# Optimization experiments

Hardware: AMD Instinct MI355X
Metric: run time of the kernel (lower is better)

The kernel has to match this reference:

```python
import jax, jax.numpy as jnp
import numpy as np

GROUPS = 3
EPS = 1e-5

def _conv(x, w, groups, pad):
    # x: NCHW, w: OIHW (grouped). pad: 'VALID' for 1x1, ((1,1),(1,1)) for 3x3 same.
    return jax.lax.conv_general_dilated(
        x, w, window_strides=(1, 1), padding=pad,
        feature_group_count=groups,
        dimension_numbers=('NCHW', 'OIHW', 'NCHW'))

def _bn(x, g, b, m, v):
    # folded inference batchnorm: y = x*scale + (beta - mean*scale)
    s = g / jnp.sqrt(v + EPS)
    return x * s[None, :, None, None] + (b - m * s)[None, :, None, None]

def _shuffle(x, groups):
    B, C, H, W = x.shape
    return x.reshape(B, groups, C // groups, H, W).transpose(0, 2, 1, 3, 4).reshape(B, C, H, W)

def setup_inputs() -> dict:
    key = jax.random.key(0)
    ks = jax.random.split(key, 16)
    B, Cin, Cout, H, W = 64, 480, 480, 28, 28
    mid = Cout // 4  # 120
    d = {}
    d['x'] = jax.random.normal(ks[0], (B, Cin, H, W), jnp.float32)
    d['w1'] = jax.random.normal(ks[1], (mid, Cin // GROUPS, 1, 1), jnp.float32) * 0.05
    d['g1'] = jax.random.uniform(ks[2], (mid,), jnp.float32)
    d['b1'] = jax.random.normal(ks[3], (mid,), jnp.float32)
    d['m1'] = jax.random.normal(ks[4], (mid,), jnp.float32)
    d['v1'] = jax.random.uniform(ks[5], (mid,), jnp.float32)
    d['w2'] = jax.random.normal(ks[6], (mid, 1, 3, 3), jnp.float32) * 0.05
    d['g2'] = jax.random.uniform(ks[7], (mid,), jnp.float32)
    d['b2'] = jax.random.normal(ks[8], (mid,), jnp.float32)
    d['m2'] = jax.random.normal(ks[9], (mid,), jnp.float32)
    d['v2'] = jax.random.uniform(ks[10], (mid,), jnp.float32)
    d['w3'] = jax.random.normal(ks[11], (Cout, mid // GROUPS, 1, 1), jnp.float32) * 0.05
    d['g3'] = jax.random.uniform(ks[12], (Cout,), jnp.float32)
    d['b3'] = jax.random.normal(ks[13], (Cout,), jnp.float32)
    d['m3'] = jax.random.normal(ks[14], (Cout,), jnp.float32)
    d['v3'] = jax.random.uniform(ks[15], (Cout,), jnp.float32)
    return d

def reference(x, w1, g1, b1, m1, v1, w2, g2, b2, m2, v2, w3, g3, b3, m3, v3):
    mid = w2.shape[0]
    shortcut = x  # in_channels == out_channels -> identity shortcut
    out = jax.nn.relu(_bn(_conv(x, w1, GROUPS, 'VALID'), g1, b1, m1, v1))
    out = _bn(_conv(out, w2, mid, ((1, 1), (1, 1))), g2, b2, m2, v2)  # depthwise 3x3
    out = _shuffle(out, GROUPS)
    out = jax.nn.relu(_bn(_conv(out, w3, GROUPS, 'VALID'), g3, b3, m3, v3))
    return out + shortcut
```

## Files before the change

kernel.cpp:

```cpp
#include <hip/hip_runtime.h>


namespace {
constexpr int CIN = 480;
constexpr int MID = 120;
constexpr int HWP = 784;
constexpr float EPSV = 1e-5f;

constexpr size_t TMP1_N = (size_t)64 * MID * HWP;
constexpr int WA1_N = 3 * 3 * 5 * 64 * 8;
constexpr int WA3_N = 3 * 10 * 2 * 64 * 8;

constexpr int S1W = 84;
constexpr int S1O = 65;
constexpr int S2O = 69;
}

typedef short bf16x8 __attribute__((ext_vector_type(8)));
typedef float f32x4  __attribute__((ext_vector_type(4)));

__device__ inline unsigned short f2bf(float v) {
    unsigned u = __float_as_uint(v);
    return (unsigned short)((u + 0x7fffu + ((u >> 16) & 1u)) >> 16);
}
__device__ inline float bf2f(unsigned s) {
    return __uint_as_float(s << 16);
}
__device__ inline void split2(float v, unsigned short& h, unsigned short& l) {
    h = f2bf(v);
    l = f2bf(v - bf2f((unsigned)h));
}

__global__ __launch_bounds__(256) void prep_k(
    const float* __restrict__ w1, const float* __restrict__ w3,
    const float* __restrict__ g1, const float* __restrict__ b1,
    const float* __restrict__ m1, const float* __restrict__ v1,
    const float* __restrict__ g2, const float* __restrict__ b2,
    const float* __restrict__ m2, const float* __restrict__ v2,
    const float* __restrict__ g3, const float* __restrict__ b3,
    const float* __restrict__ m3, const float* __restrict__ v3,
    float* __restrict__ par, unsigned short* __restrict__ wpk)
{
    const int t = blockIdx.x * 256 + threadIdx.x;
    if (t < 720) {
        if (t < 120) {
            const float s = g1[t] * rsqrtf(v1[t] + EPSV);
            par[t] = s; par[120 + t] = fmaf(-m1[t], s, b1[t]);
        } else if (t < 240) {
            const int c = t - 120;
            const float s = g2[c] * rsqrtf(v2[c] + EPSV);
            par[240 + c] = s; par[360 + c] = fmaf(-m2[c], s, b2[c]);
        } else {
            const int c = t - 240;
            const float s = g3[c] * rsqrtf(v3[c] + EPSV);
            par[480 + c] = s; par[960 + c] = fmaf(-m3[c], s, b3[c]);
        }
    } else if (t < 3600) {
        const int t1   = t - 720;
        const int lane = t1 & 63;
        const int rest = t1 >> 6;
        const int ks   = rest % 5;
        const int mtg  = rest / 5;
        const int mt   = mtg % 3;
        const int g    = mtg / 3;
        const int row  = mt * 16 + (lane & 15);
        const int k0   = ks * 32 + (lane >> 4) * 8;
        unsigned short h[8], l[8];
#pragma unroll
        for (int j = 0; j < 8; ++j) {
            float v = (row < 40) ? w1[(size_t)(g * 40 + row) * 160 + k0 + j] : 0.f;
            split2(v, h[j], l[j]);
        }
        *reinterpret_cast<uint4*>(wpk + (size_t)t1 * 8)         = *reinterpret_cast<uint4*>(h);
        *reinterpret_cast<uint4*>(wpk + WA1_N + (size_t)t1 * 8) = *reinterpret_cast<uint4*>(l);
    } else if (t < 7440) {
        const int t3   = t - 3600;
        const int lane = t3 & 63;
        const int rest = t3 >> 6;
        const int ks   = rest % 2;
        const int mtg  = rest / 2;
        const int mt   = mtg % 10;
        const int g    = mtg / 10;
        const int row  = mt * 16 + (lane & 15);
        const int k0   = ks * 32 + (lane >> 4) * 8;
        unsigned short h[8], l[8];
#pragma unroll
        for (int j = 0; j < 8; ++j) {
            const int k = k0 + j;
            float v = (k < 40) ? w3[(size_t)(g * 160 + row) * 40 + k] : 0.f;
            split2(v, h[j], l[j]);
        }
        *reinterpret_cast<uint4*>(wpk + 2 * WA1_N + (size_t)t3 * 8)         = *reinterpret_cast<uint4*>(h);
        *reinterpret_cast<uint4*>(wpk + 2 * WA1_N + WA3_N + (size_t)t3 * 8) = *reinterpret_cast<uint4*>(l);
    }
}

__global__ __launch_bounds__(256) void k1_mfma(
    const float* __restrict__ x, const unsigned short* __restrict__ wA1h,
    const float* __restrict__ par, unsigned short* __restrict__ tmp1)
{
    __shared__ __align__(16) unsigned xs32[64 * S1W];
    __shared__ float sL[40], shL[40];

    const int tid  = threadIdx.x;
    const int lane = tid & 63;
    const int wv   = tid >> 6;
    const int g    = blockIdx.y;
    const int p0   = blockIdx.x * 64;

    if (tid < 40) { sL[tid] = par[g * 40 + tid]; shL[tid] = par[120 + g * 40 + tid]; }

    const int px4s = (tid >> 4) & 15;
    {
        const int ps = p0 + px4s * 4;
        const int bs = ps / HWP;
        const int hws = ps - bs * HWP;
        const float* __restrict__ xb = x + ((size_t)bs * CIN + g * 160) * HWP + hws;

        float4 v0[5], v1[5];
#pragma unroll
        for (int i = 0; i < 5; ++i) {
            const int cp = (tid & 15) + 16 * i;
            v0[i] = *reinterpret_cast<const float4*>(xb + (size_t)(2 * cp)     * HWP);
            v1[i] = *reinterpret_cast<const float4*>(xb + (size_t)(2 * cp + 1) * HWP);
        }
#pragma unroll
        for (int i = 0; i < 5; ++i) {
            const int cp = (tid & 15) + 16 * i;
            unsigned* d = xs32 + (px4s * 4) * S1W + cp;
            d[0]       = (unsigned)f2bf(v0[i].x) | ((unsigned)f2bf(v1[i].x) << 16);
            d[S1W]     = (unsigned)f2bf(v0[i].y) | ((unsigned)f2bf(v1[i].y) << 16);
            d[2 * S1W] = (unsigned)f2bf(v0[i].z) | ((unsigned)f2bf(v1[i].z) << 16);
            d[3 * S1W] = (unsigned)f2bf(v0[i].w) | ((unsigned)f2bf(v1[i].w) << 16);
        }
    }
    __syncthreads();

    const unsigned short* __restrict__ wA1l = wA1h + WA1_N;
    const unsigned short* xsh = reinterpret_cast<const unsigned short*>(xs32);
    f32x4 acc[3];
#pragma unroll
    for (int mt = 0; mt < 3; ++mt) acc[mt] = f32x4{0.f, 0.f, 0.f, 0.f};

    const int n16 = lane & 15;
    const int kq  = lane >> 4;
    const int pxl = wv * 16 + n16;
#pragma unroll
    for (int ks = 0; ks < 5; ++ks) {
        const bf16x8 Bv = *reinterpret_cast<const bf16x8*>(
            xsh + pxl * (2 * S1W) + ks * 32 + kq * 8);
#pragma unroll
        for (int mt = 0; mt < 3; ++mt) {
            const size_t fi = (((size_t)(g * 3 + mt) * 5 + ks) * 64 + lane) * 8;
            const bf16x8 Ah = *reinterpret_cast<const bf16x8*>(wA1h + fi);
            const bf16x8 Al = *reinterpret_cast<const bf16x8*>(wA1l + fi);
            acc[mt] = __builtin_amdgcn_mfma_f32_16x16x32_bf16(Ah, Bv, acc[mt], 0, 0, 0);
            acc[mt] = __builtin_amdgcn_mfma_f32_16x16x32_bf16(Al, Bv, acc[mt], 0, 0, 0);
        }
    }
    __syncthreads();

    float* osr = reinterpret_cast<float*>(xs32);
    {
#pragma unroll
        for (int mt = 0; mt < 3; ++mt) {
#pragma unroll
            for (int r = 0; r < 4; ++r) {
                const int ocl = mt * 16 + kq * 4 + r;
                if (ocl < 40) {
                    float val = fmaf(acc[mt][r], sL[ocl], shL[ocl]);
                    osr[ocl * S1O + pxl] = val > 0.f ? val : 0.f;
                }
            }
        }
    }
    __syncthreads();

#pragma unroll
    for (int i = 0; i < 3; ++i) {
        const int task = tid + i * 256;
        if (task < 640) {
            const int ocl = task >> 4;
            const int px4 = task & 15;
            const int p   = p0 + px4 * 4;
            const int b   = p / HWP;
            const int hw  = p - b * HWP;
            const float* s = osr + ocl * S1O + px4 * 4;
            const unsigned lo = (unsigned)f2bf(s[0]) | ((unsigned)f2bf(s[1]) << 16);
            const unsigned hi = (unsigned)f2bf(s[2]) | ((unsigned)f2bf(s[3]) << 16);
            *reinterpret_cast<uint2*>(
                tmp1 + ((size_t)b * MID + g * 40 + ocl) * HWP + hw) = make_uint2(lo, hi);
        }
    }
}

__global__ __launch_bounds__(256) void k2_dw(
    const unsigned short* __restrict__ tmp1, const float* __restrict__ w2,
    const float* __restrict__ par, unsigned short* __restrict__ tmp2)
{
    __shared__ float dout[MID * S2O];
    __shared__ float w2s[1080];
    __shared__ float s2s[120], sh2s[120];

    const int tid = threadIdx.x;
    const int bx  = blockIdx.x;
    const int p0  = bx * 64;

    for (int i = tid; i < 1080; i += 256) w2s[i] = w2[i];
    if (tid < 120) { s2s[tid] = par[240 + tid]; sh2s[tid] = par[360 + tid]; }
    __syncthreads();

#pragma unroll
    for (int i = 0; i < 8; ++i) {
        const int task = tid + i * 256;
        if (task < 1920) {
            const int ch  = task >> 4;
            const int px4 = task & 15;
            const int p   = p0 + px4 * 4;
            const int b   = p / HWP;
            const int hw  = p - b * HWP;
            const int h   = hw / 28, w = hw - h * 28;
            const unsigned short* __restrict__ in = tmp1 + ((size_t)b * MID + ch) * HWP;
            const float* wk = w2s + ch * 9;

            float a0 = 0.f, a1 = 0.f, a2 = 0.f, a3 = 0.f;
#pragma unroll
            for (int dh = -1; dh <= 1; ++dh) {
                const int hh = h + dh;
                if (hh < 0 || hh > 27) continue;
                const unsigned short* r = in + hh * 28 + w;
                const uint2 cc = *reinterpret_cast<const uint2*>(r);
                const float c0 = bf2f(cc.x & 0xffffu), c1 = bf2f(cc.x >> 16);
                const float c2 = bf2f(cc.y & 0xffffu), c3 = bf2f(cc.y >> 16);
                const float cl = (w > 0)  ? bf2f(r[-1]) : 0.f;
                const float cr = (w < 24) ? bf2f(r[4])  : 0.f;
                const float* wr = wk + (dh + 1) * 3;
                a0 = fmaf(cl, wr[0], a0); a0 = fmaf(c0, wr[1], a0); a0 = fmaf(c1, wr[2], a0);
                a1 = fmaf(c0, wr[0], a1); a1 = fmaf(c1, wr[1], a1); a1 = fmaf(c2, wr[2], a1);
                a2 = fmaf(c1, wr[0], a2); a2 = fmaf(c2, wr[1], a2); a2 = fmaf(c3, wr[2], a2);
                a3 = fmaf(c2, wr[0], a3); a3 = fmaf(c3, wr[1], a3); a3 = fmaf(cr, wr[2], a3);
            }
            const float s  = s2s[ch];
            const float sh = sh2s[ch];
            const int gi = ch / 40;
            const int cs = (ch - gi * 40) * 3 + gi;
            float* d = dout + cs * S2O + px4 * 4;
            d[0] = fmaf(a0, s, sh); d[1] = fmaf(a1, s, sh);
            d[2] = fmaf(a2, s, sh); d[3] = fmaf(a3, s, sh);
        }
    }
    __syncthreads();

#pragma unroll
    for (int i = 0; i < 4; ++i) {
        const int task = tid + i * 256;
        if (task < 960) {
            const int cs  = task >> 3;
            const int px8 = task & 7;
            const int p   = p0 + px8 * 8;
            const int b   = p / HWP;
            const int hw  = p - b * HWP;
            const float* dr = dout + cs * S2O + px8 * 8;
            uint4 o;
            o.x = (unsigned)f2bf(dr[0]) | ((unsigned)f2bf(dr[1]) << 16);
            o.y = (unsigned)f2bf(dr[2]) | ((unsigned)f2bf(dr[3]) << 16);
            o.z = (unsigned)f2bf(dr[4]) | ((unsigned)f2bf(dr[5]) << 16);
            o.w = (unsigned)f2bf(dr[6]) | ((unsigned)f2bf(dr[7]) << 16);
            *reinterpret_cast<uint4*>(
                tmp2 + ((size_t)b * MID + cs) * HWP + hw) = o;
        }
    }
}

__global__ __launch_bounds__(256) void k3_mfma(
    const unsigned short* __restrict__ tmp2, const unsigned short* __restrict__ wA3h,
    const float* __restrict__ par,
    const float* __restrict__ x, float* __restrict__ out)
{
    __shared__ __align__(16) unsigned short Bfr[4096];
    __shared__ float sL[160], shL[160];

    const int tid  = threadIdx.x;
    const int lane = tid & 63;
    const int wv   = tid >> 6;
    const int bx   = blockIdx.x;
    const int gk   = blockIdx.y;
    const int p0   = bx * 64;

    if (tid < 160) {
        sL[tid]  = par[480 + gk * 160 + tid];
        shL[tid] = par[960 + gk * 160 + tid];
    }
    if (tid < 192)
        *reinterpret_cast<uint4*>(Bfr + 2560 + tid * 8) = make_uint4(0u, 0u, 0u, 0u);

#pragma unroll
    for (int i = 0; i < 3; ++i) {
        const int task = tid + i * 256;
        if (task < 640) {
            const int csl = task >> 4;
            const int px4 = task & 15;
            const int p   = p0 + px4 * 4;
            const int b   = p / HWP;
            const int hw  = p - b * HWP;
            const uint2 cc = *reinterpret_cast<const uint2*>(
                tmp2 + ((size_t)b * MID + gk * 40 + csl) * HWP + hw);
            const int kb8 = csl >> 3, j = csl & 7;
            unsigned short vals[4] = {
                (unsigned short)(cc.x & 0xffffu), (unsigned short)(cc.x >> 16),
                (unsigned short)(cc.y & 0xffffu), (unsigned short)(cc.y >> 16) };
#pragma unroll
            for (int pp = 0; pp < 4; ++pp) {
                const int px  = px4 * 4 + pp;
                const int nt  = px >> 4, n16 = px & 15;
                Bfr[((kb8 * 4 + nt) * 16 + n16) * 8 + j] = vals[pp];
            }
        }
    }

    const int n16 = lane & 15, kq = lane >> 4;
    const int pxl = wv * 16 + n16;
    const int pg  = p0 + pxl;
    const int bg  = pg / HWP;
    const int hwg = pg - bg * HWP;
    const size_t xbase = (size_t)bg * CIN * HWP + hwg;
    float xv[10][4];
#pragma unroll
    for (int mt = 0; mt < 10; ++mt) {
#pragma unroll
        for (int r = 0; r < 4; ++r) {
            const int oc = gk * 160 + mt * 16 + kq * 4 + r;
            xv[mt][r] = x[xbase + (size_t)oc * HWP];
        }
    }
    __syncthreads();

    const unsigned short* __restrict__ wA3l = wA3h + WA3_N;
    f32x4 acc[10];
#pragma unroll
    for (int mt = 0; mt < 10; ++mt) acc[mt] = f32x4{0.f, 0.f, 0.f, 0.f};

#pragma unroll
    for (int ks = 0; ks < 2; ++ks) {
        const int kb8 = ks * 4 + kq;
        const bf16x8 Bv = *reinterpret_cast<const bf16x8*>(
            Bfr + ((kb8 * 4 + wv) * 16 + n16) * 8);
#pragma unroll
        for (int mt = 0; mt < 10; ++mt) {
            const size_t fi = (((size_t)(gk * 10 + mt) * 2 + ks) * 64 + lane) * 8;
            const bf16x8 Ah = *reinterpret_cast<const bf16x8*>(wA3h + fi);
            const bf16x8 Al = *reinterpret_cast<const bf16x8*>(wA3l + fi);
            acc[mt] = __builtin_amdgcn_mfma_f32_16x16x32_bf16(Ah, Bv, acc[mt], 0, 0, 0);
            acc[mt] = __builtin_amdgcn_mfma_f32_16x16x32_bf16(Al, Bv, acc[mt], 0, 0, 0);
        }
    }

#pragma unroll
    for (int mt = 0; mt < 10; ++mt) {
#pragma unroll
        for (int r = 0; r < 4; ++r) {
            const int ocl = mt * 16 + kq * 4 + r;
            const int oc  = gk * 160 + ocl;
            float val = fmaf(acc[mt][r], sL[ocl], shL[ocl]);
            val = val > 0.f ? val : 0.f;
            out[xbase + (size_t)oc * HWP] = val + xv[mt][r];
        }
    }
}

extern "C" void kernel_launch(void* const* d_in, const int* in_sizes, int n_in,
                              void* d_out, int out_size, void* d_ws, size_t ws_size,
                              hipStream_t stream) {
    const float* x  = (const float*)d_in[0];
    const float* w1 = (const float*)d_in[1];
    const float* g1 = (const float*)d_in[2];
    const float* b1 = (const float*)d_in[3];
    const float* m1 = (const float*)d_in[4];
    const float* v1 = (const float*)d_in[5];
    const float* w2 = (const float*)d_in[6];
    const float* g2 = (const float*)d_in[7];
    const float* b2 = (const float*)d_in[8];
    const float* m2 = (const float*)d_in[9];
    const float* v2 = (const float*)d_in[10];
    const float* w3 = (const float*)d_in[11];
    const float* g3 = (const float*)d_in[12];
    const float* b3 = (const float*)d_in[13];
    const float* m3 = (const float*)d_in[14];
    const float* v3 = (const float*)d_in[15];
    float* out = (float*)d_out;

    unsigned short* tmp1 = (unsigned short*)d_ws;
    unsigned short* tmp2 = tmp1 + TMP1_N;
    float* par = (float*)(tmp2 + TMP1_N);
    unsigned short* wpk = (unsigned short*)(par + 1440);

    prep_k<<<30, 256, 0, stream>>>(w1, w3, g1, b1, m1, v1, g2, b2, m2, v2,
                                   g3, b3, m3, v3, par, wpk);
    k1_mfma<<<dim3(784, 3), 256, 0, stream>>>(x, wpk, par, tmp1);
    k2_dw  <<<784,          256, 0, stream>>>(tmp1, w2, par, tmp2);
    k3_mfma<<<dim3(784, 3), 256, 0, stream>>>(tmp2, wpk + 2 * WA1_N, par, x, out);
}
```

Before: 118.0 us.

## Stage k3 epilogue through LDS for float4 stores and split output channels

The third kernel now splits each group's 160 output channels into two halves, doubling the grid to 6 in y and halving accumulators per thread. The activated results are written to a padded LDS tile, then read back so each thread loads the residual and stores the output as float4 along pixels, instead of scalar per-element global accesses. This targets poorly vectorized epilogue traffic and register pressure, at the cost of extra LDS round trips, two more barriers, and redundant B-fragment loading across the two halves. Shared memory aliasing Bfr with the output tile is guarded by a barrier; the float4 accesses assume the 64-pixel tiles never cross a batch boundary in groups of 4.

```diff
diff --git a/kernel.cpp b/kernel.cpp
--- a/kernel.cpp
+++ b/kernel.cpp
@@ -14,6 +14,7 @@
 constexpr int S1W = 84;
 constexpr int S1O = 65;
 constexpr int S2O = 69;
+constexpr int S3O = 67;
 }
 
 typedef short bf16x8 __attribute__((ext_vector_type(8)));
@@ -277,19 +278,22 @@
     const float* __restrict__ par,
     const float* __restrict__ x, float* __restrict__ out)
 {
-    __shared__ __align__(16) unsigned short Bfr[4096];
-    __shared__ float sL[160], shL[160];
+    __shared__ __align__(16) float uni[80 * S3O];
+    __shared__ float sL[80], shL[80];
+    unsigned short* Bfr = reinterpret_cast<unsigned short*>(uni);
+    float* osr = uni;
 
     const int tid  = threadIdx.x;
     const int lane = tid & 63;
     const int wv   = tid >> 6;
     const int bx   = blockIdx.x;
-    const int gk   = blockIdx.y;
+    const int g    = blockIdx.y >> 1;
+    const int mh   = blockIdx.y & 1;
     const int p0   = bx * 64;
 
-    if (tid < 160) {
-        sL[tid]  = par[480 + gk * 160 + tid];
-        shL[tid] = par[960 + gk * 160 + tid];
+    if (tid < 80) {
+        sL[tid]  = par[480 + g * 160 + mh * 80 + tid];
+        shL[tid] = par[960 + g * 160 + mh * 80 + tid];
     }
     if (tid < 192)
         *reinterpret_cast<uint4*>(Bfr + 2560 + tid * 8) = make_uint4(0u, 0u, 0u, 0u);
@@ -304,7 +308,7 @@
             const int b   = p / HWP;
             const int hw  = p - b * HWP;
             const uint2 cc = *reinterpret_cast<const uint2*>(
-                tmp2 + ((size_t)b * MID + gk * 40 + csl) * HWP + hw);
+                tmp2 + ((size_t)b * MID + g * 40 + csl) * HWP + hw);
             const int kb8 = csl >> 3, j = csl & 7;
             unsigned short vals[4] = {
                 (unsigned short)(cc.x & 0xffffu), (unsigned short)(cc.x >> 16),
@@ -317,54 +321,61 @@
             }
         }
     }
-
-    const int n16 = lane & 15, kq = lane >> 4;
-    const int pxl = wv * 16 + n16;
-    const int pg  = p0 + pxl;
-    const int bg  = pg / HWP;
-    const int hwg = pg - bg * HWP;
-    const size_t xbase = (size_t)bg * CIN * HWP + hwg;
-    float xv[10][4];
-#pragma unroll
-    for (int mt = 0; mt < 10; ++mt) {
-#pragma unroll
-        for (int r = 0; r < 4; ++r) {
-            const int oc = gk * 160 + mt * 16 + kq * 4 + r;
-            xv[mt][r] = x[xbase + (size_t)oc * HWP];
-        }
-    }
     __syncthreads();
 
     const unsigned short* __restrict__ wA3l = wA3h + WA3_N;
-    f32x4 acc[10];
-#pragma unroll
-    for (int mt = 0; mt < 10; ++mt) acc[mt] = f32x4{0.f, 0.f, 0.f, 0.f};
-
+    const int nt = wv;
+    f32x4 acc[5];
+#pragma unroll
+    for (int mt = 0; mt < 5; ++mt) acc[mt] = f32x4{0.f, 0.f, 0.f, 0.f};
+
+    const int kq = lane >> 4, n16l = lane & 15;
 #pragma unroll
     for (int ks = 0; ks < 2; ++ks) {
         const int kb8 = ks * 4 + kq;
         const bf16x8 Bv = *reinterpret_cast<const bf16x8*>(
-            Bfr + ((kb8 * 4 + wv) * 16 + n16) * 8);
-#pragma unroll
-        for (int mt = 0; mt < 10; ++mt) {
-            const size_t fi = (((size_t)(gk * 10 + mt) * 2 + ks) * 64 + lane) * 8;
+            Bfr + ((kb8 * 4 + nt) * 16 + n16l) * 8);
+#pragma unroll
+        for (int mt = 0; mt < 5; ++mt) {
+            const size_t fi = (((size_t)(g * 10 + mh * 5 + mt) * 2 + ks) * 64 + lane) * 8;
             const bf16x8 Ah = *reinterpret_cast<const bf16x8*>(wA3h + fi);
             const bf16x8 Al = *reinterpret_cast<const bf16x8*>(wA3l + fi);
             acc[mt] = __builtin_amdgcn_mfma_f32_16x16x32_bf16(Ah, Bv, acc[mt], 0, 0, 0);
             acc[mt] = __builtin_amdgcn_mfma_f32_16x16x32_bf16(Al, Bv, acc[mt], 0, 0, 0);
         }
     }
-
-#pragma unroll
-    for (int mt = 0; mt < 10; ++mt) {
-#pragma unroll
-        for (int r = 0; r < 4; ++r) {
-            const int ocl = mt * 16 + kq * 4 + r;
-            const int oc  = gk * 160 + ocl;
-            float val = fmaf(acc[mt][r], sL[ocl], shL[ocl]);
-            val = val > 0.f ? val : 0.f;
-            out[xbase + (size_t)oc * HWP] = val + xv[mt][r];
-        }
+    __syncthreads();
+
+    {
+        const int pxl = nt * 16 + n16l;
+#pragma unroll
+        for (int mt = 0; mt < 5; ++mt) {
+#pragma unroll
+            for (int r = 0; r < 4; ++r) {
+                const int ocl = mt * 16 + kq * 4 + r;
+                float val = fmaf(acc[mt][r], sL[ocl], shL[ocl]);
+                osr[ocl * S3O + pxl] = val > 0.f ? val : 0.f;
+            }
+        }
+    }
+    __syncthreads();
+
+#pragma unroll
+    for (int i = 0; i < 5; ++i) {
+        const int task = tid + i * 256;
+        const int ocl  = task >> 4;
+        const int px4  = task & 15;
+        const int p    = p0 + px4 * 4;
+        const int b    = p / HWP;
+        const int hw   = p - b * HWP;
+        const int oc   = g * 160 + mh * 80 + ocl;
+        const size_t idx = ((size_t)b * CIN + oc) * HWP + hw;
+        const float* s = osr + ocl * S3O + px4 * 4;
+        const float4 sc = *reinterpret_cast<const float4*>(x + idx);
+        float4 o;
+        o.x = s[0] + sc.x; o.y = s[1] + sc.y;
+        o.z = s[2] + sc.z; o.w = s[3] + sc.w;
+        *reinterpret_cast<float4*>(out + idx) = o;
     }
 }
 
@@ -398,5 +409,5 @@
                                    g3, b3, m3, v3, par, wpk);
     k1_mfma<<<dim3(784, 3), 256, 0, stream>>>(x, wpk, par, tmp1);
     k2_dw  <<<784,          256, 0, stream>>>(tmp1, w2, par, tmp2);
-    k3_mfma<<<dim3(784, 3), 256, 0, stream>>>(tmp2, wpk + 2 * WA1_N, par, x, out);
-}
+    k3_mfma<<<dim3(784, 6), 256, 0, stream>>>(tmp2, wpk + 2 * WA1_N, par, x, out);
+}
```

After: 99.61 us. -15.6%, faster.
